# Performance work log

Measured on AMD Instinct MI355X. Metric: run time of the kernel, lower is better.

## Reference

```python
import jax, jax.numpy as jnp
import numpy as np

N = 100000
E = 3200000
NFEAT, NHID, NCLASS = 512, 64, 64
K = 10
ALPHA = 0.1


def setup_inputs() -> dict:
    key = jax.random.key(0)
    ks = jax.random.split(key, 8)
    x = jax.random.normal(ks[0], (N, NFEAT), dtype=jnp.float32)
    edge_index = jax.random.randint(ks[1], (2, E), 0, N, dtype=jnp.int32)
    s1 = 1.0 / np.sqrt(NFEAT)
    W1 = jax.random.uniform(ks[2], (NFEAT, NHID), jnp.float32, -s1, s1)
    b1 = jax.random.uniform(ks[3], (NHID,), jnp.float32, -s1, s1)
    s2 = 1.0 / np.sqrt(NHID)
    W2 = jax.random.uniform(ks[4], (NHID, NCLASS), jnp.float32, -s2, s2)
    b2 = jax.random.uniform(ks[5], (NCLASS,), jnp.float32, -s2, s2)
    # PPR init of gamma coefficients: temp[k] = alpha*(1-alpha)^k, temp[K] = (1-alpha)^K
    temp = ALPHA * (1.0 - ALPHA) ** np.arange(K + 1)
    temp[-1] = (1.0 - ALPHA) ** K
    temp = jnp.asarray(temp, dtype=jnp.float32)
    return {"x": x, "edge_index": edge_index, "W1": W1, "b1": b1, "W2": W2, "b2": b2, "temp": temp}


def _gcn_norm(edge_index, num_nodes):
    # add self loops, weight 1 (PyG gcn_norm defaults)
    loop = jnp.arange(num_nodes, dtype=edge_index.dtype)
    src = jnp.concatenate([edge_index[0], loop])
    dst = jnp.concatenate([edge_index[1], loop])
    w = jnp.ones(src.shape[0], dtype=jnp.float32)
    deg = jax.ops.segment_sum(w, dst, num_segments=num_nodes)
    dinv = jnp.where(deg > 0, jax.lax.rsqrt(deg), 0.0)
    norm = dinv[src] * w * dinv[dst]
    return src, dst, norm


def reference(x, edge_index, W1, b1, W2, b2, temp):
    # MLP part (eval mode, dropout is identity)
    h = jax.nn.relu(x @ W1 + b1) @ W2 + b2  # [N, nclass]
    src, dst, norm = _gcn_norm(edge_index, x.shape[0])
    hidden = h * temp[0]
    for k in range(K):
        # gather-scale-scatter: h <- A_hat @ h
        h = jax.ops.segment_sum(norm[:, None] * h[src], dst, num_segments=x.shape[0])
        hidden = hidden + temp[k + 1] * h
    return hidden
```

## Files before the change

kernel.cpp:

```cpp
#include <hip/hip_runtime.h>

static constexpr int N = 100000;
static constexpr int E = 3200000;
static constexpr int NFEAT = 512;
static constexpr int K = 10;

typedef _Float16 half8 __attribute__((ext_vector_type(8)));
typedef _Float16 half4v __attribute__((ext_vector_type(4)));

static constexpr size_t OFF_CNT    = 0;
static constexpr size_t OFF_FILL   = 512ull * 1024;
static constexpr size_t OFF_ROWPTR = 1024ull * 1024;
static constexpr size_t OFF_DINV   = 1536ull * 1024;
static constexpr size_t OFF_BSUM   = 2048ull * 1024;
static constexpr size_t OFF_EW     = 2560ull * 1024;
static constexpr size_t OFF_GA     = OFF_EW + (size_t)E * 4 + 1024;
static constexpr size_t OFF_GB     = OFF_GA + (size_t)N * 64 * 2 + 1024;
static constexpr size_t OFF_H1     = OFF_GB + (size_t)N * 64 * 2 + 1024;

__global__ __launch_bounds__(256) void count_k(const int* __restrict__ dst,
                                               int* __restrict__ cnt) {
  int e = blockIdx.x * 256 + threadIdx.x;
  if (e < E) atomicAdd(&cnt[dst[e]], 1);
}

__global__ __launch_bounds__(256) void dinv_k(const int* __restrict__ cnt,
                                              float* __restrict__ dinv) {
  int i = blockIdx.x * 256 + threadIdx.x;
  if (i < N) dinv[i] = 1.0f / sqrtf((float)(cnt[i] + 1));
}

__device__ inline int wave_incl_scan(int x) {
  int lane = threadIdx.x & 63;
#pragma unroll
  for (int off = 1; off < 64; off <<= 1) {
    int y = __shfl_up(x, off, 64);
    if (lane >= off) x += y;
  }
  return x;
}

__global__ __launch_bounds__(256) void scan1_k(const int* __restrict__ cnt,
                                               int* __restrict__ rowptr,
                                               int* __restrict__ bsum) {
  __shared__ int wsum[4];
  int tid = threadIdx.x, wid = tid >> 6, lane = tid & 63;
  int base = blockIdx.x * 1024 + tid * 4;
  int4 v = {0, 0, 0, 0};
  if (base + 3 < N) {
    v = *(const int4*)(cnt + base);
  } else {
    if (base + 0 < N) v.x = cnt[base + 0];
    if (base + 1 < N) v.y = cnt[base + 1];
    if (base + 2 < N) v.z = cnt[base + 2];
    if (base + 3 < N) v.w = cnt[base + 3];
  }
  int tsum = v.x + v.y + v.z + v.w;
  int incl = wave_incl_scan(tsum);
  if (lane == 63) wsum[wid] = incl;
  __syncthreads();
  int wof = 0;
  for (int i = 0; i < wid; ++i) wof += wsum[i];
  int e0 = wof + incl - tsum;
  if (base + 0 < N) rowptr[base + 0] = e0;
  if (base + 1 < N) rowptr[base + 1] = e0 + v.x;
  if (base + 2 < N) rowptr[base + 2] = e0 + v.x + v.y;
  if (base + 3 < N) rowptr[base + 3] = e0 + v.x + v.y + v.z;
  if (tid == 255) bsum[blockIdx.x] = wof + incl;
}

__global__ __launch_bounds__(128) void scan2_k(int* __restrict__ bsum) {
  __shared__ int w0sum;
  int tid = threadIdx.x, wid = tid >> 6, lane = tid & 63;
  int v = (tid < 98) ? bsum[tid] : 0;
  int incl = wave_incl_scan(v);
  if (wid == 0 && lane == 63) w0sum = incl;
  __syncthreads();
  int excl = incl - v + (wid ? w0sum : 0);
  if (tid < 98) bsum[tid] = excl;
}

__global__ __launch_bounds__(256) void scan3_k(int* __restrict__ rowptr,
                                               const int* __restrict__ bsum) {
  int i = blockIdx.x * 256 + threadIdx.x;
  if (i < N) rowptr[i] += bsum[blockIdx.x >> 2];
  if (i == 0) rowptr[N] = E;
}

__global__ __launch_bounds__(256) void fill2_k(const int* __restrict__ src,
                                               const int* __restrict__ dst,
                                               const int* __restrict__ rowptr,
                                               int* __restrict__ fillc,
                                               int* __restrict__ ew) {
  const int slice = blockIdx.x & 7;
  const int chunk = blockIdx.x >> 3;
  const int lo = slice * 12500;
  const int hi = lo + 12500;
  int e = chunk * 4096 + threadIdx.x;
  const int eend = min(E, chunk * 4096 + 4096);
  for (; e < eend; e += 256) {
    int d = dst[e];
    if (d >= lo && d < hi) {
      int pos = rowptr[d] + atomicAdd(&fillc[d], 1);
      ew[pos] = src[e];
    }
  }
}

__global__ __launch_bounds__(256) void gemm1_k(const float* __restrict__ x,
                                               const float* __restrict__ W1,
                                               const float* __restrict__ b1,
                                               float* __restrict__ h1) {
  __shared__ float xs[16][256];
  __shared__ float w1s[16 * 64];
  const int tid = threadIdx.x;
  const int n0 = blockIdx.x * 256;
  const int tn = tid & 127;
  const int jh = tid >> 7;
  float4 acca[8], accb[8];
#pragma unroll
  for (int i = 0; i < 8; ++i) {
    acca[i] = float4{0.f, 0.f, 0.f, 0.f};
    accb[i] = float4{0.f, 0.f, 0.f, 0.f};
  }
  const int rowA = min(n0 + tid, N - 1);
  const float* xr = x + (size_t)rowA * NFEAT;
  for (int k0 = 0; k0 < NFEAT; k0 += 16) {
    float4 a0 = *(const float4*)(xr + k0 + 0);
    float4 a1 = *(const float4*)(xr + k0 + 4);
    float4 a2 = *(const float4*)(xr + k0 + 8);
    float4 a3 = *(const float4*)(xr + k0 + 12);
    float4 wv = *(const float4*)(W1 + (size_t)k0 * 64 + tid * 4);
    __syncthreads();
    xs[0][tid] = a0.x;  xs[1][tid] = a0.y;  xs[2][tid] = a0.z;  xs[3][tid] = a0.w;
    xs[4][tid] = a1.x;  xs[5][tid] = a1.y;  xs[6][tid] = a1.z;  xs[7][tid] = a1.w;
    xs[8][tid] = a2.x;  xs[9][tid] = a2.y;  xs[10][tid] = a2.z; xs[11][tid] = a2.w;
    xs[12][tid] = a3.x; xs[13][tid] = a3.y; xs[14][tid] = a3.z; xs[15][tid] = a3.w;
    *(float4*)&w1s[tid * 4] = wv;
    __syncthreads();
#pragma unroll
    for (int kk = 0; kk < 16; ++kk) {
      float xa = xs[kk][tn];
      float xb = xs[kk][tn + 128];
      const float* wr = &w1s[kk * 64 + jh * 32];
#pragma unroll
      for (int jj = 0; jj < 8; ++jj) {
        float4 w4 = *(const float4*)(wr + jj * 4);
        acca[jj].x += xa * w4.x; acca[jj].y += xa * w4.y;
        acca[jj].z += xa * w4.z; acca[jj].w += xa * w4.w;
        accb[jj].x += xb * w4.x; accb[jj].y += xb * w4.y;
        accb[jj].z += xb * w4.z; accb[jj].w += xb * w4.w;
      }
    }
  }
  const int na = n0 + tn, nb = na + 128;
#pragma unroll
  for (int jj = 0; jj < 8; ++jj) {
    int j = jh * 32 + jj * 4;
    float4 bb = *(const float4*)(b1 + j);
    float4 ra, rb;
    ra.x = fmaxf(acca[jj].x + bb.x, 0.f); ra.y = fmaxf(acca[jj].y + bb.y, 0.f);
    ra.z = fmaxf(acca[jj].z + bb.z, 0.f); ra.w = fmaxf(acca[jj].w + bb.w, 0.f);
    rb.x = fmaxf(accb[jj].x + bb.x, 0.f); rb.y = fmaxf(accb[jj].y + bb.y, 0.f);
    rb.z = fmaxf(accb[jj].z + bb.z, 0.f); rb.w = fmaxf(accb[jj].w + bb.w, 0.f);
    if (na < N) *(float4*)(h1 + (size_t)na * 64 + j) = ra;
    if (nb < N) *(float4*)(h1 + (size_t)nb * 64 + j) = rb;
  }
}

__global__ __launch_bounds__(256) void gemm2_k(const float* __restrict__ h1,
                                               const float* __restrict__ W2,
                                               const float* __restrict__ b2,
                                               const float* __restrict__ temp,
                                               const float* __restrict__ dinv,
                                               _Float16* __restrict__ g0,
                                               float* __restrict__ out) {
  __shared__ float w2s[64 * 64];
  const int tid = threadIdx.x;
#pragma unroll
  for (int i = 0; i < 4; ++i)
    *(float4*)&w2s[(i * 256 + tid) * 4] = *(const float4*)(W2 + (size_t)(i * 256 + tid) * 4);
  __syncthreads();
  const int node = blockIdx.x * 256 + tid;
  if (node >= N) return;
  float4 acc[16];
#pragma unroll
  for (int c = 0; c < 16; ++c) acc[c] = *(const float4*)(b2 + c * 4);
  const float* hr = h1 + (size_t)node * 64;
  for (int j0 = 0; j0 < 64; j0 += 4) {
    float4 hv = *(const float4*)(hr + j0);
    float hv4[4] = {hv.x, hv.y, hv.z, hv.w};
#pragma unroll
    for (int l = 0; l < 4; ++l) {
      const float* wr = &w2s[(j0 + l) * 64];
#pragma unroll
      for (int c = 0; c < 16; ++c) {
        float4 w4 = *(const float4*)(wr + c * 4);
        acc[c].x += hv4[l] * w4.x; acc[c].y += hv4[l] * w4.y;
        acc[c].z += hv4[l] * w4.z; acc[c].w += hv4[l] * w4.w;
      }
    }
  }
  const float t0 = temp[0];
  const float di = dinv[node];
  _Float16* gp = g0 + (size_t)node * 64;
  float* op = out + (size_t)node * 64;
#pragma unroll
  for (int c = 0; c < 16; ++c) {
    float4 o;
    o.x = t0 * acc[c].x; o.y = t0 * acc[c].y;
    o.z = t0 * acc[c].z; o.w = t0 * acc[c].w;
    *(float4*)(op + c * 4) = o;
    half4v g;
    g[0] = (_Float16)(di * acc[c].x); g[1] = (_Float16)(di * acc[c].y);
    g[2] = (_Float16)(di * acc[c].z); g[3] = (_Float16)(di * acc[c].w);
    *(half4v*)(gp + c * 4) = g;
  }
}

__global__ __launch_bounds__(256) void prop_k(const _Float16* __restrict__ gin,
                                              _Float16* __restrict__ gout,
                                              float* __restrict__ out,
                                              const int* __restrict__ rowptr,
                                              const int* __restrict__ es,
                                              const float* __restrict__ dinv,
                                              const float* __restrict__ temp,
                                              int kp1, int writeh) {
  const int tid = threadIdx.x;
  const int sub = tid >> 3;
  const int l = tid & 7;
  const int node = blockIdx.x * 32 + sub;
  const int rs = rowptr[node];
  const int re = rowptr[node + 1];
  const float di = dinv[node];
  const _Float16* __restrict__ gq = gin + l * 8;

  half8 sr = *(const half8*)(gq + (size_t)node * 64);
  float a0[8], a1[8], a2[8], a3[8];
#pragma unroll
  for (int i = 0; i < 8; ++i) {
    a0[i] = (float)sr[i];
    a1[i] = 0.f; a2[i] = 0.f; a3[i] = 0.f;
  }

  int e = rs;
  for (; e + 4 <= re; e += 4) {
    int s0 = es[e], s1 = es[e + 1], s2 = es[e + 2], s3 = es[e + 3];
    half8 r0 = *(const half8*)(gq + (size_t)s0 * 64);
    half8 r1 = *(const half8*)(gq + (size_t)s1 * 64);
    half8 r2 = *(const half8*)(gq + (size_t)s2 * 64);
    half8 r3 = *(const half8*)(gq + (size_t)s3 * 64);
#pragma unroll
    for (int i = 0; i < 8; ++i) {
      a0[i] += (float)r0[i];
      a1[i] += (float)r1[i];
      a2[i] += (float)r2[i];
      a3[i] += (float)r3[i];
    }
  }
  for (; e < re; ++e) {
    int s0 = es[e];
    half8 r0 = *(const half8*)(gq + (size_t)s0 * 64);
#pragma unroll
    for (int i = 0; i < 8; ++i) a0[i] += (float)r0[i];
  }

  float S[8];
#pragma unroll
  for (int i = 0; i < 8; ++i) S[i] = (a0[i] + a1[i]) + (a2[i] + a3[i]);

  const float th = temp[kp1] * di;
  const float dd = di * di;
  const size_t base = (size_t)node * 64 + l * 8;
  float4 o0 = *(const float4*)(out + base);
  float4 o1 = *(const float4*)(out + base + 4);
  o0.x += th * S[0]; o0.y += th * S[1]; o0.z += th * S[2]; o0.w += th * S[3];
  o1.x += th * S[4]; o1.y += th * S[5]; o1.z += th * S[6]; o1.w += th * S[7];
  *(float4*)(out + base) = o0;
  *(float4*)(out + base + 4) = o1;
  if (writeh) {
    half8 gw;
#pragma unroll
    for (int i = 0; i < 8; ++i) gw[i] = (_Float16)(dd * S[i]);
    *(half8*)(gout + base) = gw;
  }
}

extern "C" void kernel_launch(void* const* d_in, const int* in_sizes, int n_in,
                              void* d_out, int out_size, void* d_ws, size_t ws_size,
                              hipStream_t stream) {
  const float* x = (const float*)d_in[0];
  const int* ei = (const int*)d_in[1];
  const float* W1 = (const float*)d_in[2];
  const float* b1 = (const float*)d_in[3];
  const float* W2 = (const float*)d_in[4];
  const float* b2 = (const float*)d_in[5];
  const float* temp = (const float*)d_in[6];
  const int* srcp = ei;
  const int* dstp = ei + E;

  unsigned char* ws = (unsigned char*)d_ws;
  int* cnt = (int*)(ws + OFF_CNT);
  int* fillc = (int*)(ws + OFF_FILL);
  int* rowptr = (int*)(ws + OFF_ROWPTR);
  float* dinv = (float*)(ws + OFF_DINV);
  int* bsum = (int*)(ws + OFF_BSUM);
  int* es = (int*)(ws + OFF_EW);
  _Float16* gA = (_Float16*)(ws + OFF_GA);
  _Float16* gB = (_Float16*)(ws + OFF_GB);
  float* h1 = (float*)(ws + OFF_H1);
  float* out = (float*)d_out;

  hipMemsetAsync(cnt, 0, (size_t)N * 4, stream);
  hipMemsetAsync(fillc, 0, (size_t)N * 4, stream);

  count_k<<<E / 256, 256, 0, stream>>>(dstp, cnt);
  dinv_k<<<(N + 255) / 256, 256, 0, stream>>>(cnt, dinv);
  scan1_k<<<(N + 1023) / 1024, 256, 0, stream>>>(cnt, rowptr, bsum);
  scan2_k<<<1, 128, 0, stream>>>(bsum);
  scan3_k<<<(N + 255) / 256, 256, 0, stream>>>(rowptr, bsum);
  fill2_k<<<8 * 782, 256, 0, stream>>>(srcp, dstp, rowptr, fillc, es);

  gemm1_k<<<(N + 255) / 256, 256, 0, stream>>>(x, W1, b1, h1);
  gemm2_k<<<(N + 255) / 256, 256, 0, stream>>>(h1, W2, b2, temp, dinv, gA, out);

  const _Float16* gin = gA;
  _Float16* gout = gB;
  for (int k = 0; k < K; ++k) {
    prop_k<<<N / 32, 256, 0, stream>>>(gin, gout, out, rowptr, es, dinv, temp,
                                       k + 1, (k + 1 < K) ? 1 : 0);
    _Float16* t = (_Float16*)gin;
    gin = gout;
    gout = t;
  }
}
```

Measured before the change: 1.076 ms.

## Split propagation features into four 16-column quarters for cache-resident gathers

The propagation state and output accumulator move into four feature-quarter planes of 16 columns each. Each propagation step now runs as four launches, one per quarter, so the gathered working set (N*16 halves, about 3.2MB) can stay in cache and the random gathers hit it more often. In exchange the edge list is reread four times per step, there are more launches, and a merge kernel is added to rebuild the row-major output. The change also stores h1 in fp16 and adds nontemporal loads and stores on streaming index and output accesses.

```diff
diff --git a/kernel.cpp b/kernel.cpp
--- a/kernel.cpp
+++ b/kernel.cpp
@@ -4,9 +4,11 @@
 static constexpr int E = 3200000;
 static constexpr int NFEAT = 512;
 static constexpr int K = 10;
+static constexpr int QSTRIDE = N * 16;
 
 typedef _Float16 half8 __attribute__((ext_vector_type(8)));
 typedef _Float16 half4v __attribute__((ext_vector_type(4)));
+typedef float float4nt __attribute__((ext_vector_type(4)));
 
 static constexpr size_t OFF_CNT    = 0;
 static constexpr size_t OFF_FILL   = 512ull * 1024;
@@ -16,12 +18,13 @@
 static constexpr size_t OFF_EW     = 2560ull * 1024;
 static constexpr size_t OFF_GA     = OFF_EW + (size_t)E * 4 + 1024;
 static constexpr size_t OFF_GB     = OFF_GA + (size_t)N * 64 * 2 + 1024;
-static constexpr size_t OFF_H1     = OFF_GB + (size_t)N * 64 * 2 + 1024;
+static constexpr size_t OFF_OUTQ   = OFF_GB + (size_t)N * 64 * 2 + 1024;
+static constexpr size_t OFF_H1     = OFF_OUTQ + (size_t)N * 64 * 4 + 1024;
 
 __global__ __launch_bounds__(256) void count_k(const int* __restrict__ dst,
                                                int* __restrict__ cnt) {
   int e = blockIdx.x * 256 + threadIdx.x;
-  if (e < E) atomicAdd(&cnt[dst[e]], 1);
+  if (e < E) atomicAdd(&cnt[__builtin_nontemporal_load(dst + e)], 1);
 }
 
 __global__ __launch_bounds__(256) void dinv_k(const int* __restrict__ cnt,
@@ -91,7 +94,7 @@
                                                const int* __restrict__ dst,
                                                const int* __restrict__ rowptr,
                                                int* __restrict__ fillc,
-                                               int* __restrict__ ew) {
+                                               int* __restrict__ es) {
   const int slice = blockIdx.x & 7;
   const int chunk = blockIdx.x >> 3;
   const int lo = slice * 12500;
@@ -99,10 +102,10 @@
   int e = chunk * 4096 + threadIdx.x;
   const int eend = min(E, chunk * 4096 + 4096);
   for (; e < eend; e += 256) {
-    int d = dst[e];
+    int d = __builtin_nontemporal_load(dst + e);
     if (d >= lo && d < hi) {
       int pos = rowptr[d] + atomicAdd(&fillc[d], 1);
-      ew[pos] = src[e];
+      es[pos] = __builtin_nontemporal_load(src + e);
     }
   }
 }
@@ -110,7 +113,7 @@
 __global__ __launch_bounds__(256) void gemm1_k(const float* __restrict__ x,
                                                const float* __restrict__ W1,
                                                const float* __restrict__ b1,
-                                               float* __restrict__ h1) {
+                                               _Float16* __restrict__ h1) {
   __shared__ float xs[16][256];
   __shared__ float w1s[16 * 64];
   const int tid = threadIdx.x;
@@ -158,23 +161,27 @@
   for (int jj = 0; jj < 8; ++jj) {
     int j = jh * 32 + jj * 4;
     float4 bb = *(const float4*)(b1 + j);
-    float4 ra, rb;
-    ra.x = fmaxf(acca[jj].x + bb.x, 0.f); ra.y = fmaxf(acca[jj].y + bb.y, 0.f);
-    ra.z = fmaxf(acca[jj].z + bb.z, 0.f); ra.w = fmaxf(acca[jj].w + bb.w, 0.f);
-    rb.x = fmaxf(accb[jj].x + bb.x, 0.f); rb.y = fmaxf(accb[jj].y + bb.y, 0.f);
-    rb.z = fmaxf(accb[jj].z + bb.z, 0.f); rb.w = fmaxf(accb[jj].w + bb.w, 0.f);
-    if (na < N) *(float4*)(h1 + (size_t)na * 64 + j) = ra;
-    if (nb < N) *(float4*)(h1 + (size_t)nb * 64 + j) = rb;
-  }
-}
-
-__global__ __launch_bounds__(256) void gemm2_k(const float* __restrict__ h1,
+    half4v ra, rb;
+    ra[0] = (_Float16)fmaxf(acca[jj].x + bb.x, 0.f);
+    ra[1] = (_Float16)fmaxf(acca[jj].y + bb.y, 0.f);
+    ra[2] = (_Float16)fmaxf(acca[jj].z + bb.z, 0.f);
+    ra[3] = (_Float16)fmaxf(acca[jj].w + bb.w, 0.f);
+    rb[0] = (_Float16)fmaxf(accb[jj].x + bb.x, 0.f);
+    rb[1] = (_Float16)fmaxf(accb[jj].y + bb.y, 0.f);
+    rb[2] = (_Float16)fmaxf(accb[jj].z + bb.z, 0.f);
+    rb[3] = (_Float16)fmaxf(accb[jj].w + bb.w, 0.f);
+    if (na < N) *(half4v*)(h1 + (size_t)na * 64 + j) = ra;
+    if (nb < N) *(half4v*)(h1 + (size_t)nb * 64 + j) = rb;
+  }
+}
+
+__global__ __launch_bounds__(256) void gemm2_k(const _Float16* __restrict__ h1,
                                                const float* __restrict__ W2,
                                                const float* __restrict__ b2,
                                                const float* __restrict__ temp,
                                                const float* __restrict__ dinv,
                                                _Float16* __restrict__ g0,
-                                               float* __restrict__ out) {
+                                               float* __restrict__ outq) {
   __shared__ float w2s[64 * 64];
   const int tid = threadIdx.x;
 #pragma unroll
@@ -186,56 +193,59 @@
   float4 acc[16];
 #pragma unroll
   for (int c = 0; c < 16; ++c) acc[c] = *(const float4*)(b2 + c * 4);
-  const float* hr = h1 + (size_t)node * 64;
-  for (int j0 = 0; j0 < 64; j0 += 4) {
-    float4 hv = *(const float4*)(hr + j0);
-    float hv4[4] = {hv.x, hv.y, hv.z, hv.w};
-#pragma unroll
-    for (int l = 0; l < 4; ++l) {
+  const _Float16* hr = h1 + (size_t)node * 64;
+  for (int j0 = 0; j0 < 64; j0 += 8) {
+    half8 hv = *(const half8*)(hr + j0);
+#pragma unroll
+    for (int l = 0; l < 8; ++l) {
+      float hl = (float)hv[l];
       const float* wr = &w2s[(j0 + l) * 64];
 #pragma unroll
       for (int c = 0; c < 16; ++c) {
         float4 w4 = *(const float4*)(wr + c * 4);
-        acc[c].x += hv4[l] * w4.x; acc[c].y += hv4[l] * w4.y;
-        acc[c].z += hv4[l] * w4.z; acc[c].w += hv4[l] * w4.w;
+        acc[c].x += hl * w4.x; acc[c].y += hl * w4.y;
+        acc[c].z += hl * w4.z; acc[c].w += hl * w4.w;
       }
     }
   }
   const float t0 = temp[0];
   const float di = dinv[node];
-  _Float16* gp = g0 + (size_t)node * 64;
-  float* op = out + (size_t)node * 64;
-#pragma unroll
-  for (int c = 0; c < 16; ++c) {
-    float4 o;
-    o.x = t0 * acc[c].x; o.y = t0 * acc[c].y;
-    o.z = t0 * acc[c].z; o.w = t0 * acc[c].w;
-    *(float4*)(op + c * 4) = o;
-    half4v g;
-    g[0] = (_Float16)(di * acc[c].x); g[1] = (_Float16)(di * acc[c].y);
-    g[2] = (_Float16)(di * acc[c].z); g[3] = (_Float16)(di * acc[c].w);
-    *(half4v*)(gp + c * 4) = g;
-  }
-}
-
-__global__ __launch_bounds__(256) void prop_k(const _Float16* __restrict__ gin,
-                                              _Float16* __restrict__ gout,
-                                              float* __restrict__ out,
-                                              const int* __restrict__ rowptr,
-                                              const int* __restrict__ es,
-                                              const float* __restrict__ dinv,
-                                              const float* __restrict__ temp,
-                                              int kp1, int writeh) {
+#pragma unroll
+  for (int q = 0; q < 4; ++q) {
+    float* oqp = outq + (size_t)q * QSTRIDE + (size_t)node * 16;
+    _Float16* gqp = g0 + (size_t)q * QSTRIDE + (size_t)node * 16;
+#pragma unroll
+    for (int c2 = 0; c2 < 4; ++c2) {
+      const float4 a = acc[q * 4 + c2];
+      float4 o;
+      o.x = t0 * a.x; o.y = t0 * a.y; o.z = t0 * a.z; o.w = t0 * a.w;
+      *(float4*)(oqp + c2 * 4) = o;
+      half4v g;
+      g[0] = (_Float16)(di * a.x); g[1] = (_Float16)(di * a.y);
+      g[2] = (_Float16)(di * a.z); g[3] = (_Float16)(di * a.w);
+      *(half4v*)(gqp + c2 * 4) = g;
+    }
+  }
+}
+
+__global__ __launch_bounds__(256) void propq_k(const _Float16* __restrict__ gin,
+                                               _Float16* __restrict__ gout,
+                                               float* __restrict__ outq,
+                                               const int* __restrict__ rowptr,
+                                               const int* __restrict__ es,
+                                               const float* __restrict__ dinv,
+                                               const float* __restrict__ temp,
+                                               int kp1, int writeh) {
   const int tid = threadIdx.x;
-  const int sub = tid >> 3;
-  const int l = tid & 7;
-  const int node = blockIdx.x * 32 + sub;
+  const int node = blockIdx.x * 128 + (tid >> 1);
+  if (node >= N) return;
+  const int l = tid & 1;
   const int rs = rowptr[node];
   const int re = rowptr[node + 1];
   const float di = dinv[node];
   const _Float16* __restrict__ gq = gin + l * 8;
 
-  half8 sr = *(const half8*)(gq + (size_t)node * 64);
+  half8 sr = *(const half8*)(gq + (size_t)node * 16);
   float a0[8], a1[8], a2[8], a3[8];
 #pragma unroll
   for (int i = 0; i < 8; ++i) {
@@ -245,11 +255,14 @@
 
   int e = rs;
   for (; e + 4 <= re; e += 4) {
-    int s0 = es[e], s1 = es[e + 1], s2 = es[e + 2], s3 = es[e + 3];
-    half8 r0 = *(const half8*)(gq + (size_t)s0 * 64);
-    half8 r1 = *(const half8*)(gq + (size_t)s1 * 64);
-    half8 r2 = *(const half8*)(gq + (size_t)s2 * 64);
-    half8 r3 = *(const half8*)(gq + (size_t)s3 * 64);
+    int s0 = __builtin_nontemporal_load(es + e);
+    int s1 = __builtin_nontemporal_load(es + e + 1);
+    int s2 = __builtin_nontemporal_load(es + e + 2);
+    int s3 = __builtin_nontemporal_load(es + e + 3);
+    half8 r0 = *(const half8*)(gq + (size_t)s0 * 16);
+    half8 r1 = *(const half8*)(gq + (size_t)s1 * 16);
+    half8 r2 = *(const half8*)(gq + (size_t)s2 * 16);
+    half8 r3 = *(const half8*)(gq + (size_t)s3 * 16);
 #pragma unroll
     for (int i = 0; i < 8; ++i) {
       a0[i] += (float)r0[i];
@@ -259,8 +272,8 @@
     }
   }
   for (; e < re; ++e) {
-    int s0 = es[e];
-    half8 r0 = *(const half8*)(gq + (size_t)s0 * 64);
+    int s0 = __builtin_nontemporal_load(es + e);
+    half8 r0 = *(const half8*)(gq + (size_t)s0 * 16);
 #pragma unroll
     for (int i = 0; i < 8; ++i) a0[i] += (float)r0[i];
   }
@@ -271,19 +284,30 @@
 
   const float th = temp[kp1] * di;
   const float dd = di * di;
-  const size_t base = (size_t)node * 64 + l * 8;
-  float4 o0 = *(const float4*)(out + base);
-  float4 o1 = *(const float4*)(out + base + 4);
+  const size_t base = (size_t)node * 16 + l * 8;
+  float4nt o0 = __builtin_nontemporal_load((const float4nt*)(outq + base));
+  float4nt o1 = __builtin_nontemporal_load((const float4nt*)(outq + base + 4));
   o0.x += th * S[0]; o0.y += th * S[1]; o0.z += th * S[2]; o0.w += th * S[3];
   o1.x += th * S[4]; o1.y += th * S[5]; o1.z += th * S[6]; o1.w += th * S[7];
-  *(float4*)(out + base) = o0;
-  *(float4*)(out + base + 4) = o1;
+  __builtin_nontemporal_store(o0, (float4nt*)(outq + base));
+  __builtin_nontemporal_store(o1, (float4nt*)(outq + base + 4));
   if (writeh) {
     half8 gw;
 #pragma unroll
     for (int i = 0; i < 8; ++i) gw[i] = (_Float16)(dd * S[i]);
     *(half8*)(gout + base) = gw;
   }
+}
+
+__global__ __launch_bounds__(256) void merge_k(const float* __restrict__ outq,
+                                               float* __restrict__ out) {
+  int i = blockIdx.x * 256 + threadIdx.x;
+  if (i >= N * 16) return;
+  int node = i >> 4;
+  int fq = i & 15;
+  float4nt v = __builtin_nontemporal_load(
+      (const float4nt*)(outq + (size_t)(fq >> 2) * QSTRIDE + (size_t)node * 16 + (fq & 3) * 4));
+  ((float4nt*)out)[i] = v;
 }
 
 extern "C" void kernel_launch(void* const* d_in, const int* in_sizes, int n_in,
@@ -308,7 +332,8 @@
   int* es = (int*)(ws + OFF_EW);
   _Float16* gA = (_Float16*)(ws + OFF_GA);
   _Float16* gB = (_Float16*)(ws + OFF_GB);
-  float* h1 = (float*)(ws + OFF_H1);
+  float* outq = (float*)(ws + OFF_OUTQ);
+  _Float16* h1 = (_Float16*)(ws + OFF_H1);
   float* out = (float*)d_out;
 
   hipMemsetAsync(cnt, 0, (size_t)N * 4, stream);
@@ -322,15 +347,22 @@
   fill2_k<<<8 * 782, 256, 0, stream>>>(srcp, dstp, rowptr, fillc, es);
 
   gemm1_k<<<(N + 255) / 256, 256, 0, stream>>>(x, W1, b1, h1);
-  gemm2_k<<<(N + 255) / 256, 256, 0, stream>>>(h1, W2, b2, temp, dinv, gA, out);
+  gemm2_k<<<(N + 255) / 256, 256, 0, stream>>>(h1, W2, b2, temp, dinv, gA, outq);
 
   const _Float16* gin = gA;
   _Float16* gout = gB;
+  const int nblk = (N + 127) / 128;
   for (int k = 0; k < K; ++k) {
-    prop_k<<<N / 32, 256, 0, stream>>>(gin, gout, out, rowptr, es, dinv, temp,
-                                       k + 1, (k + 1 < K) ? 1 : 0);
+    const int wh = (k + 1 < K) ? 1 : 0;
+    for (int q = 0; q < 4; ++q) {
+      propq_k<<<nblk, 256, 0, stream>>>(gin + (size_t)q * QSTRIDE,
+                                        gout + (size_t)q * QSTRIDE,
+                                        outq + (size_t)q * QSTRIDE,
+                                        rowptr, es, dinv, temp, k + 1, wh);
+    }
     _Float16* t = (_Float16*)gin;
     gin = gout;
     gout = t;
   }
-}
+  merge_k<<<(N * 16 + 255) / 256, 256, 0, stream>>>(outq, out);
+}
```

Measured after the change: 2.212 ms. 2.05x slower.

## Store propagation state in per-row-scaled FP8 and the hidden layer in FP16

Applied to the files above, without the earlier changes.

The propagated feature state moves from fp16 to fp8 with one float scale per node, computed from a row max reduced across the 8 lanes that own the row. Steps 2 to 10 gather 64-byte rows instead of 128-byte rows, cutting random-gather traffic, and the first step still reads the fp16 output of gemm2. The MLP hidden activations h1 are also stored as fp16, and the edge-list loads in the CSR-building kernels become nontemporal. The cost is an extra scale gather per edge, the conversion instructions, and much lower precision accumulated over ten hops, which may break the accuracy tolerance.

```diff
diff --git a/kernel.cpp b/kernel.cpp
--- a/kernel.cpp
+++ b/kernel.cpp
@@ -7,6 +7,8 @@
 
 typedef _Float16 half8 __attribute__((ext_vector_type(8)));
 typedef _Float16 half4v __attribute__((ext_vector_type(4)));
+typedef float v2f __attribute__((ext_vector_type(2)));
+typedef unsigned int uint2v __attribute__((ext_vector_type(2)));
 
 static constexpr size_t OFF_CNT    = 0;
 static constexpr size_t OFF_FILL   = 512ull * 1024;
@@ -14,14 +16,17 @@
 static constexpr size_t OFF_DINV   = 1536ull * 1024;
 static constexpr size_t OFF_BSUM   = 2048ull * 1024;
 static constexpr size_t OFF_EW     = 2560ull * 1024;
-static constexpr size_t OFF_GA     = OFF_EW + (size_t)E * 4 + 1024;
-static constexpr size_t OFF_GB     = OFF_GA + (size_t)N * 64 * 2 + 1024;
-static constexpr size_t OFF_H1     = OFF_GB + (size_t)N * 64 * 2 + 1024;
+static constexpr size_t OFF_G16    = OFF_EW + (size_t)E * 4 + 1024;
+static constexpr size_t OFF_GA     = OFF_G16 + (size_t)N * 64 * 2 + 1024;
+static constexpr size_t OFF_GB     = OFF_GA + (size_t)N * 64 + 1024;
+static constexpr size_t OFF_SCA    = OFF_GB + (size_t)N * 64 + 1024;
+static constexpr size_t OFF_SCB    = OFF_SCA + (size_t)N * 4 + 1024;
+static constexpr size_t OFF_H1     = OFF_SCB + (size_t)N * 4 + 1024;
 
 __global__ __launch_bounds__(256) void count_k(const int* __restrict__ dst,
                                                int* __restrict__ cnt) {
   int e = blockIdx.x * 256 + threadIdx.x;
-  if (e < E) atomicAdd(&cnt[dst[e]], 1);
+  if (e < E) atomicAdd(&cnt[__builtin_nontemporal_load(dst + e)], 1);
 }
 
 __global__ __launch_bounds__(256) void dinv_k(const int* __restrict__ cnt,
@@ -91,7 +96,7 @@
                                                const int* __restrict__ dst,
                                                const int* __restrict__ rowptr,
                                                int* __restrict__ fillc,
-                                               int* __restrict__ ew) {
+                                               int* __restrict__ es) {
   const int slice = blockIdx.x & 7;
   const int chunk = blockIdx.x >> 3;
   const int lo = slice * 12500;
@@ -99,10 +104,10 @@
   int e = chunk * 4096 + threadIdx.x;
   const int eend = min(E, chunk * 4096 + 4096);
   for (; e < eend; e += 256) {
-    int d = dst[e];
+    int d = __builtin_nontemporal_load(dst + e);
     if (d >= lo && d < hi) {
       int pos = rowptr[d] + atomicAdd(&fillc[d], 1);
-      ew[pos] = src[e];
+      es[pos] = __builtin_nontemporal_load(src + e);
     }
   }
 }
@@ -110,7 +115,7 @@
 __global__ __launch_bounds__(256) void gemm1_k(const float* __restrict__ x,
                                                const float* __restrict__ W1,
                                                const float* __restrict__ b1,
-                                               float* __restrict__ h1) {
+                                               _Float16* __restrict__ h1) {
   __shared__ float xs[16][256];
   __shared__ float w1s[16 * 64];
   const int tid = threadIdx.x;
@@ -158,22 +163,26 @@
   for (int jj = 0; jj < 8; ++jj) {
     int j = jh * 32 + jj * 4;
     float4 bb = *(const float4*)(b1 + j);
-    float4 ra, rb;
-    ra.x = fmaxf(acca[jj].x + bb.x, 0.f); ra.y = fmaxf(acca[jj].y + bb.y, 0.f);
-    ra.z = fmaxf(acca[jj].z + bb.z, 0.f); ra.w = fmaxf(acca[jj].w + bb.w, 0.f);
-    rb.x = fmaxf(accb[jj].x + bb.x, 0.f); rb.y = fmaxf(accb[jj].y + bb.y, 0.f);
-    rb.z = fmaxf(accb[jj].z + bb.z, 0.f); rb.w = fmaxf(accb[jj].w + bb.w, 0.f);
-    if (na < N) *(float4*)(h1 + (size_t)na * 64 + j) = ra;
-    if (nb < N) *(float4*)(h1 + (size_t)nb * 64 + j) = rb;
-  }
-}
-
-__global__ __launch_bounds__(256) void gemm2_k(const float* __restrict__ h1,
+    half4v ra, rb;
+    ra[0] = (_Float16)fmaxf(acca[jj].x + bb.x, 0.f);
+    ra[1] = (_Float16)fmaxf(acca[jj].y + bb.y, 0.f);
+    ra[2] = (_Float16)fmaxf(acca[jj].z + bb.z, 0.f);
+    ra[3] = (_Float16)fmaxf(acca[jj].w + bb.w, 0.f);
+    rb[0] = (_Float16)fmaxf(accb[jj].x + bb.x, 0.f);
+    rb[1] = (_Float16)fmaxf(accb[jj].y + bb.y, 0.f);
+    rb[2] = (_Float16)fmaxf(accb[jj].z + bb.z, 0.f);
+    rb[3] = (_Float16)fmaxf(accb[jj].w + bb.w, 0.f);
+    if (na < N) *(half4v*)(h1 + (size_t)na * 64 + j) = ra;
+    if (nb < N) *(half4v*)(h1 + (size_t)nb * 64 + j) = rb;
+  }
+}
+
+__global__ __launch_bounds__(256) void gemm2_k(const _Float16* __restrict__ h1,
                                                const float* __restrict__ W2,
                                                const float* __restrict__ b2,
                                                const float* __restrict__ temp,
                                                const float* __restrict__ dinv,
-                                               _Float16* __restrict__ g0,
+                                               _Float16* __restrict__ g16,
                                                float* __restrict__ out) {
   __shared__ float w2s[64 * 64];
   const int tid = threadIdx.x;
@@ -186,46 +195,77 @@
   float4 acc[16];
 #pragma unroll
   for (int c = 0; c < 16; ++c) acc[c] = *(const float4*)(b2 + c * 4);
-  const float* hr = h1 + (size_t)node * 64;
-  for (int j0 = 0; j0 < 64; j0 += 4) {
-    float4 hv = *(const float4*)(hr + j0);
-    float hv4[4] = {hv.x, hv.y, hv.z, hv.w};
-#pragma unroll
-    for (int l = 0; l < 4; ++l) {
+  const _Float16* hr = h1 + (size_t)node * 64;
+  for (int j0 = 0; j0 < 64; j0 += 8) {
+    half8 hv = *(const half8*)(hr + j0);
+#pragma unroll
+    for (int l = 0; l < 8; ++l) {
+      float hl = (float)hv[l];
       const float* wr = &w2s[(j0 + l) * 64];
 #pragma unroll
       for (int c = 0; c < 16; ++c) {
         float4 w4 = *(const float4*)(wr + c * 4);
-        acc[c].x += hv4[l] * w4.x; acc[c].y += hv4[l] * w4.y;
-        acc[c].z += hv4[l] * w4.z; acc[c].w += hv4[l] * w4.w;
+        acc[c].x += hl * w4.x; acc[c].y += hl * w4.y;
+        acc[c].z += hl * w4.z; acc[c].w += hl * w4.w;
       }
     }
   }
   const float t0 = temp[0];
   const float di = dinv[node];
-  _Float16* gp = g0 + (size_t)node * 64;
   float* op = out + (size_t)node * 64;
+  _Float16* gp = g16 + (size_t)node * 64;
 #pragma unroll
   for (int c = 0; c < 16; ++c) {
+    const float4 a = acc[c];
     float4 o;
-    o.x = t0 * acc[c].x; o.y = t0 * acc[c].y;
-    o.z = t0 * acc[c].z; o.w = t0 * acc[c].w;
+    o.x = t0 * a.x; o.y = t0 * a.y; o.z = t0 * a.z; o.w = t0 * a.w;
     *(float4*)(op + c * 4) = o;
     half4v g;
-    g[0] = (_Float16)(di * acc[c].x); g[1] = (_Float16)(di * acc[c].y);
-    g[2] = (_Float16)(di * acc[c].z); g[3] = (_Float16)(di * acc[c].w);
+    g[0] = (_Float16)(di * a.x); g[1] = (_Float16)(di * a.y);
+    g[2] = (_Float16)(di * a.z); g[3] = (_Float16)(di * a.w);
     *(half4v*)(gp + c * 4) = g;
   }
 }
 
-__global__ __launch_bounds__(256) void prop_k(const _Float16* __restrict__ gin,
-                                              _Float16* __restrict__ gout,
-                                              float* __restrict__ out,
-                                              const int* __restrict__ rowptr,
-                                              const int* __restrict__ es,
-                                              const float* __restrict__ dinv,
-                                              const float* __restrict__ temp,
-                                              int kp1, int writeh) {
+__device__ inline void dec8(uint2v u, float* f) {
+  v2f p0 = __builtin_amdgcn_cvt_pk_f32_fp8(u.x, false);
+  v2f p1 = __builtin_amdgcn_cvt_pk_f32_fp8(u.x, true);
+  v2f p2 = __builtin_amdgcn_cvt_pk_f32_fp8(u.y, false);
+  v2f p3 = __builtin_amdgcn_cvt_pk_f32_fp8(u.y, true);
+  f[0] = p0.x; f[1] = p0.y; f[2] = p1.x; f[3] = p1.y;
+  f[4] = p2.x; f[5] = p2.y; f[6] = p3.x; f[7] = p3.y;
+}
+
+__device__ inline void write_fp8_state(const float* S, float dd, int node, int l,
+                                       unsigned int* __restrict__ gout,
+                                       float* __restrict__ oscale) {
+  float v[8];
+#pragma unroll
+  for (int i = 0; i < 8; ++i) v[i] = dd * S[i];
+  float m = 0.f;
+#pragma unroll
+  for (int i = 0; i < 8; ++i) m = fmaxf(m, fabsf(v[i]));
+#pragma unroll
+  for (int off = 1; off < 8; off <<= 1) m = fmaxf(m, __shfl_xor(m, off, 64));
+  const float esc = (m > 0.f) ? 240.0f / m : 0.f;
+  if (l == 0) oscale[node] = m * (1.0f / 240.0f);
+  unsigned int w0 = 0, w1 = 0;
+  w0 = __builtin_amdgcn_cvt_pk_fp8_f32(v[0] * esc, v[1] * esc, w0, false);
+  w0 = __builtin_amdgcn_cvt_pk_fp8_f32(v[2] * esc, v[3] * esc, w0, true);
+  w1 = __builtin_amdgcn_cvt_pk_fp8_f32(v[4] * esc, v[5] * esc, w1, false);
+  w1 = __builtin_amdgcn_cvt_pk_fp8_f32(v[6] * esc, v[7] * esc, w1, true);
+  uint2v gw; gw.x = w0; gw.y = w1;
+  *(uint2v*)(gout + (size_t)node * 16 + l * 2) = gw;
+}
+
+__global__ __launch_bounds__(256) void prop16_k(const _Float16* __restrict__ gin,
+                                                unsigned int* __restrict__ gout,
+                                                float* __restrict__ oscale,
+                                                float* __restrict__ out,
+                                                const int* __restrict__ rowptr,
+                                                const int* __restrict__ es,
+                                                const float* __restrict__ dinv,
+                                                const float* __restrict__ temp) {
   const int tid = threadIdx.x;
   const int sub = tid >> 3;
   const int l = tid & 7;
@@ -263,6 +303,80 @@
     half8 r0 = *(const half8*)(gq + (size_t)s0 * 64);
 #pragma unroll
     for (int i = 0; i < 8; ++i) a0[i] += (float)r0[i];
+  }
+
+  float S[8];
+#pragma unroll
+  for (int i = 0; i < 8; ++i) S[i] = (a0[i] + a1[i]) + (a2[i] + a3[i]);
+
+  const float th = temp[1] * di;
+  const float dd = di * di;
+  const size_t base = (size_t)node * 64 + l * 8;
+  float4 o0 = *(const float4*)(out + base);
+  float4 o1 = *(const float4*)(out + base + 4);
+  o0.x += th * S[0]; o0.y += th * S[1]; o0.z += th * S[2]; o0.w += th * S[3];
+  o1.x += th * S[4]; o1.y += th * S[5]; o1.z += th * S[6]; o1.w += th * S[7];
+  *(float4*)(out + base) = o0;
+  *(float4*)(out + base + 4) = o1;
+  write_fp8_state(S, dd, node, l, gout, oscale);
+}
+
+__global__ __launch_bounds__(256) void prop8_k(const unsigned int* __restrict__ gin,
+                                               const float* __restrict__ iscale,
+                                               unsigned int* __restrict__ gout,
+                                               float* __restrict__ oscale,
+                                               float* __restrict__ out,
+                                               const int* __restrict__ rowptr,
+                                               const int* __restrict__ es,
+                                               const float* __restrict__ dinv,
+                                               const float* __restrict__ temp,
+                                               int kp1, int writeh) {
+  const int tid = threadIdx.x;
+  const int sub = tid >> 3;
+  const int l = tid & 7;
+  const int node = blockIdx.x * 32 + sub;
+  const int rs = rowptr[node];
+  const int re = rowptr[node + 1];
+  const float di = dinv[node];
+  const unsigned int* __restrict__ gq = gin + l * 2;
+
+  uint2v sv = *(const uint2v*)(gq + (size_t)node * 16);
+  const float sci = iscale[node];
+  float t8[8];
+  dec8(sv, t8);
+  float a0[8], a1[8], a2[8], a3[8];
+#pragma unroll
+  for (int i = 0; i < 8; ++i) {
+    a0[i] = sci * t8[i];
+    a1[i] = 0.f; a2[i] = 0.f; a3[i] = 0.f;
+  }
+
+  int e = rs;
+  for (; e + 4 <= re; e += 4) {
+    int s0 = es[e], s1 = es[e + 1], s2 = es[e + 2], s3 = es[e + 3];
+    float sc0 = iscale[s0], sc1 = iscale[s1], sc2 = iscale[s2], sc3 = iscale[s3];
+    uint2v u0 = *(const uint2v*)(gq + (size_t)s0 * 16);
+    uint2v u1 = *(const uint2v*)(gq + (size_t)s1 * 16);
+    uint2v u2 = *(const uint2v*)(gq + (size_t)s2 * 16);
+    uint2v u3 = *(const uint2v*)(gq + (size_t)s3 * 16);
+    float r0[8], r1[8], r2[8], r3[8];
+    dec8(u0, r0); dec8(u1, r1); dec8(u2, r2); dec8(u3, r3);
+#pragma unroll
+    for (int i = 0; i < 8; ++i) {
+      a0[i] += sc0 * r0[i];
+      a1[i] += sc1 * r1[i];
+      a2[i] += sc2 * r2[i];
+      a3[i] += sc3 * r3[i];
+    }
+  }
+  for (; e < re; ++e) {
+    int s0 = es[e];
+    float sc0 = iscale[s0];
+    uint2v u0 = *(const uint2v*)(gq + (size_t)s0 * 16);
+    float r0[8];
+    dec8(u0, r0);
+#pragma unroll
+    for (int i = 0; i < 8; ++i) a0[i] += sc0 * r0[i];
   }
 
   float S[8];
@@ -278,12 +392,7 @@
   o1.x += th * S[4]; o1.y += th * S[5]; o1.z += th * S[6]; o1.w += th * S[7];
   *(float4*)(out + base) = o0;
   *(float4*)(out + base + 4) = o1;
-  if (writeh) {
-    half8 gw;
-#pragma unroll
-    for (int i = 0; i < 8; ++i) gw[i] = (_Float16)(dd * S[i]);
-    *(half8*)(gout + base) = gw;
-  }
+  if (writeh) write_fp8_state(S, dd, node, l, gout, oscale);
 }
 
 extern "C" void kernel_launch(void* const* d_in, const int* in_sizes, int n_in,
@@ -306,9 +415,12 @@
   float* dinv = (float*)(ws + OFF_DINV);
   int* bsum = (int*)(ws + OFF_BSUM);
   int* es = (int*)(ws + OFF_EW);
-  _Float16* gA = (_Float16*)(ws + OFF_GA);
-  _Float16* gB = (_Float16*)(ws + OFF_GB);
-  float* h1 = (float*)(ws + OFF_H1);
+  _Float16* g16 = (_Float16*)(ws + OFF_G16);
+  unsigned int* gA = (unsigned int*)(ws + OFF_GA);
+  unsigned int* gB = (unsigned int*)(ws + OFF_GB);
+  float* scA = (float*)(ws + OFF_SCA);
+  float* scB = (float*)(ws + OFF_SCB);
+  _Float16* h1 = (_Float16*)(ws + OFF_H1);
   float* out = (float*)d_out;
 
   hipMemsetAsync(cnt, 0, (size_t)N * 4, stream);
@@ -322,15 +434,18 @@
   fill2_k<<<8 * 782, 256, 0, stream>>>(srcp, dstp, rowptr, fillc, es);
 
   gemm1_k<<<(N + 255) / 256, 256, 0, stream>>>(x, W1, b1, h1);
-  gemm2_k<<<(N + 255) / 256, 256, 0, stream>>>(h1, W2, b2, temp, dinv, gA, out);
-
-  const _Float16* gin = gA;
-  _Float16* gout = gB;
-  for (int k = 0; k < K; ++k) {
-    prop_k<<<N / 32, 256, 0, stream>>>(gin, gout, out, rowptr, es, dinv, temp,
-                                       k + 1, (k + 1 < K) ? 1 : 0);
-    _Float16* t = (_Float16*)gin;
-    gin = gout;
-    gout = t;
-  }
-}
+  gemm2_k<<<(N + 255) / 256, 256, 0, stream>>>(h1, W2, b2, temp, dinv, g16, out);
+
+  prop16_k<<<N / 32, 256, 0, stream>>>(g16, gA, scA, out, rowptr, es, dinv, temp);
+
+  const unsigned int* gin = gA;
+  unsigned int* gout = gB;
+  const float* sin = scA;
+  float* sout = scB;
+  for (int k = 1; k < K; ++k) {
+    prop8_k<<<N / 32, 256, 0, stream>>>(gin, sin, gout, sout, out, rowptr, es,
+                                        dinv, temp, k + 1, (k + 1 < K) ? 1 : 0);
+    const unsigned int* tg = gin; gin = gout; gout = (unsigned int*)tg;
+    const float* ts = sin; sin = sout; sout = (float*)ts;
+  }
+}
```

After: 1.026 ms. 4.6% less time.
